# Optimization experiments

Measured on AMD Instinct MI355X. Metric: run time of the kernel, lower is better.

Reference implementation:

```python
import jax, jax.numpy as jnp
import numpy as np

LR = 0.01
EPS = 1e-10


def setup_inputs() -> dict:
    key = jax.random.key(0)
    k1, k2, k3, k4 = jax.random.split(key, 4)
    N, V, D = 262144, 1000000, 64
    idx = jax.random.randint(k1, (N,), 0, V, dtype=jnp.int64 if jax.config.jax_enable_x64 else jnp.int32)
    grad = jax.random.normal(k2, (N, D), dtype=jnp.float32)
    state = jax.random.uniform(k3, (V, D), dtype=jnp.float32)  # accumulated squared grads (>=0)
    emb = jax.random.normal(k4, (V, D), dtype=jnp.float32)
    return {"idx": idx, "grad": grad, "state": state, "emb": emb}


def reference(idx, grad, state, emb):
    N, D = grad.shape
    V = state.shape[0]
    # unique + segment-mean of grads per unique index (torch.unique + index_add / counts)
    # fixed-size unique for jit; padded slots get fill_value=V (out of range -> dropped on scatter)
    uniq, inverse, counts = jnp.unique(idx, return_inverse=True, return_counts=True,
                                       size=N, fill_value=V)
    grad_sum = jnp.zeros((N, D), dtype=grad.dtype).at[inverse].add(grad)
    grad_values = grad_sum / jnp.maximum(counts, 1)[:, None].astype(grad.dtype)
    # gather state rows (padded rows clip-gather but their writes are dropped)
    state_value = state[jnp.minimum(uniq, V - 1)] + grad_values * grad_values
    new_state = state.at[uniq].set(state_value, mode='drop')
    std_values = jnp.sqrt(state_value) + EPS
    new_emb = emb.at[uniq].add(-(LR * grad_values / std_values), mode='drop')
    return new_state, new_emb
```

## Files before the change

### kernel.cpp

```cpp
#include <hip/hip_runtime.h>

#define LR 0.01f
#define EPS 1e-10f


__global__ void init_head_kernel(int* __restrict__ head, int V) {
    int i = blockIdx.x * blockDim.x + threadIdx.x;
    if (i < V) head[i] = -1;
}

__global__ void link_kernel(const int* __restrict__ idx,
                            int* __restrict__ head,
                            int* __restrict__ next, int N) {
    int i = blockIdx.x * blockDim.x + threadIdx.x;
    if (i >= N) return;
    next[i] = atomicExch(&head[idx[i]], i);
}

__global__ void fused_kernel(const float* __restrict__ state,
                             const float* __restrict__ emb,
                             const float* __restrict__ grad,
                             const int* __restrict__ head,
                             const int* __restrict__ next,
                             float* __restrict__ out_state,
                             float* __restrict__ out_emb, int V) {
    long long t = (long long)blockIdx.x * blockDim.x + threadIdx.x;
    long long row = t >> 4;
    int q = (int)(t & 15);
    if (row >= V) return;
    size_t off = (size_t)row * 64 + (size_t)q * 4;

    int h = head[row];
    float4 s = *reinterpret_cast<const float4*>(state + off);
    float4 e = *reinterpret_cast<const float4*>(emb + off);

    if (h < 0) {
        *reinterpret_cast<float4*>(out_state + off) = s;
        *reinterpret_cast<float4*>(out_emb + off) = e;
        return;
    }

    float sum0 = 0.f, sum1 = 0.f, sum2 = 0.f, sum3 = 0.f;
    int c = 0;
    for (int j = h; j >= 0; j = next[j]) {
        const float4 g = *reinterpret_cast<const float4*>(grad + (size_t)j * 64 + (size_t)q * 4);
        sum0 += g.x; sum1 += g.y; sum2 += g.z; sum3 += g.w;
        ++c;
    }
    float inv = 1.0f / (float)c;
    float m0 = sum0 * inv, m1 = sum1 * inv, m2 = sum2 * inv, m3 = sum3 * inv;
    float s0 = s.x + m0 * m0, s1 = s.y + m1 * m1;
    float s2 = s.z + m2 * m2, s3 = s.w + m3 * m3;
    float4 ns = make_float4(s0, s1, s2, s3);
    float4 ne = make_float4(e.x - LR * m0 / (sqrtf(s0) + EPS),
                            e.y - LR * m1 / (sqrtf(s1) + EPS),
                            e.z - LR * m2 / (sqrtf(s2) + EPS),
                            e.w - LR * m3 / (sqrtf(s3) + EPS));
    *reinterpret_cast<float4*>(out_state + off) = ns;
    *reinterpret_cast<float4*>(out_emb + off) = ne;
}

extern "C" void kernel_launch(void* const* d_in, const int* in_sizes, int n_in,
                              void* d_out, int out_size, void* d_ws, size_t ws_size,
                              hipStream_t stream) {
    const int* idx = (const int*)d_in[0];
    const float* grad = (const float*)d_in[1];
    const float* state = (const float*)d_in[2];
    const float* emb = (const float*)d_in[3];

    int N = in_sizes[0];
    int D = in_sizes[1] / N;
    long long VD = in_sizes[2];
    int V = (int)(VD / D);

    float* out_state = (float*)d_out;
    float* out_emb = (float*)d_out + (size_t)V * D;
    int* head = (int*)d_ws;
    int* next = (int*)d_ws + V;

    const int threads = 256;

    init_head_kernel<<<(V + threads - 1) / threads, threads, 0, stream>>>(head, V);

    link_kernel<<<(N + threads - 1) / threads, threads, 0, stream>>>(idx, head, next, N);

    {
        long long work = (long long)V * 16;
        int blocks = (int)((work + threads - 1) / threads);
        fused_kernel<<<blocks, threads, 0, stream>>>(state, emb, grad, head, next,
                                                     out_state, out_emb, V);
    }
}
```

Before: 214.4 us.

## Use nontemporal loads/stores, grid-stride loop, and memset for head init

Replaces the head-initialisation kernel with hipMemsetAsync. The fused kernel becomes a grid-stride loop with a fixed 4096 blocks. The early-exit branch for untouched rows is removed in favour of a branchless path guarded by c>0. State and embedding rows now use nontemporal vector loads and stores so the streaming traffic does not pollute cache. The aim is to cut launch overhead and cache thrash on a bandwidth-bound pass. The risks are that the fixed grid under-occupies the GPU and that nontemporal hints may not help.

```diff
diff --git a/kernel.cpp b/kernel.cpp
--- a/kernel.cpp
+++ b/kernel.cpp
@@ -3,11 +3,8 @@
 #define LR 0.01f
 #define EPS 1e-10f
 
+typedef float f32x4 __attribute__((ext_vector_type(4)));
 
-__global__ void init_head_kernel(int* __restrict__ head, int V) {
-    int i = blockIdx.x * blockDim.x + threadIdx.x;
-    if (i < V) head[i] = -1;
-}
 
 __global__ void link_kernel(const int* __restrict__ idx,
                             int* __restrict__ head,
@@ -23,41 +20,37 @@
                              const int* __restrict__ head,
                              const int* __restrict__ next,
                              float* __restrict__ out_state,
-                             float* __restrict__ out_emb, int V) {
-    long long t = (long long)blockIdx.x * blockDim.x + threadIdx.x;
-    long long row = t >> 4;
-    int q = (int)(t & 15);
-    if (row >= V) return;
-    size_t off = (size_t)row * 64 + (size_t)q * 4;
+                             float* __restrict__ out_emb, long long total) {
+    long long stride = (long long)gridDim.x * blockDim.x;
+    for (long long t = (long long)blockIdx.x * blockDim.x + threadIdx.x;
+         t < total; t += stride) {
+        long long row = t >> 4;
+        int q = (int)(t & 15);
+        size_t off = (size_t)row * 64 + (size_t)q * 4;
 
-    int h = head[row];
-    float4 s = *reinterpret_cast<const float4*>(state + off);
-    float4 e = *reinterpret_cast<const float4*>(emb + off);
+        int h = head[row];
+        f32x4 s = __builtin_nontemporal_load(reinterpret_cast<const f32x4*>(state + off));
+        f32x4 e = __builtin_nontemporal_load(reinterpret_cast<const f32x4*>(emb + off));
 
-    if (h < 0) {
-        *reinterpret_cast<float4*>(out_state + off) = s;
-        *reinterpret_cast<float4*>(out_emb + off) = e;
-        return;
+        float sum0 = 0.f, sum1 = 0.f, sum2 = 0.f, sum3 = 0.f;
+        int c = 0;
+        for (int j = h; j >= 0; j = next[j]) {
+            const f32x4 g = *reinterpret_cast<const f32x4*>(grad + (size_t)j * 64 + (size_t)q * 4);
+            sum0 += g.x; sum1 += g.y; sum2 += g.z; sum3 += g.w;
+            ++c;
+        }
+        float inv = (c > 0) ? (1.0f / (float)c) : 0.0f;
+        float m0 = sum0 * inv, m1 = sum1 * inv, m2 = sum2 * inv, m3 = sum3 * inv;
+        float s0 = s.x + m0 * m0, s1 = s.y + m1 * m1;
+        float s2 = s.z + m2 * m2, s3 = s.w + m3 * m3;
+        f32x4 ns = { s0, s1, s2, s3 };
+        f32x4 ne = { e.x - LR * m0 / (sqrtf(s0) + EPS),
+                     e.y - LR * m1 / (sqrtf(s1) + EPS),
+                     e.z - LR * m2 / (sqrtf(s2) + EPS),
+                     e.w - LR * m3 / (sqrtf(s3) + EPS) };
+        __builtin_nontemporal_store(ns, reinterpret_cast<f32x4*>(out_state + off));
+        __builtin_nontemporal_store(ne, reinterpret_cast<f32x4*>(out_emb + off));
     }
-
-    float sum0 = 0.f, sum1 = 0.f, sum2 = 0.f, sum3 = 0.f;
-    int c = 0;
-    for (int j = h; j >= 0; j = next[j]) {
-        const float4 g = *reinterpret_cast<const float4*>(grad + (size_t)j * 64 + (size_t)q * 4);
-        sum0 += g.x; sum1 += g.y; sum2 += g.z; sum3 += g.w;
-        ++c;
-    }
-    float inv = 1.0f / (float)c;
-    float m0 = sum0 * inv, m1 = sum1 * inv, m2 = sum2 * inv, m3 = sum3 * inv;
-    float s0 = s.x + m0 * m0, s1 = s.y + m1 * m1;
-    float s2 = s.z + m2 * m2, s3 = s.w + m3 * m3;
-    float4 ns = make_float4(s0, s1, s2, s3);
-    float4 ne = make_float4(e.x - LR * m0 / (sqrtf(s0) + EPS),
-                            e.y - LR * m1 / (sqrtf(s1) + EPS),
-                            e.z - LR * m2 / (sqrtf(s2) + EPS),
-                            e.w - LR * m3 / (sqrtf(s3) + EPS));
-    *reinterpret_cast<float4*>(out_state + off) = ns;
-    *reinterpret_cast<float4*>(out_emb + off) = ne;
 }
 
 extern "C" void kernel_launch(void* const* d_in, const int* in_sizes, int n_in,
@@ -80,14 +73,14 @@
 
     const int threads = 256;
 
-    init_head_kernel<<<(V + threads - 1) / threads, threads, 0, stream>>>(head, V);
+    (void)hipMemsetAsync(head, 0xFF, (size_t)V * sizeof(int), stream);
 
     link_kernel<<<(N + threads - 1) / threads, threads, 0, stream>>>(idx, head, next, N);
 
     {
-        long long work = (long long)V * 16;
-        int blocks = (int)((work + threads - 1) / threads);
+        long long total = (long long)V * 16;
+        int blocks = 4096;
         fused_kernel<<<blocks, threads, 0, stream>>>(state, emb, grad, head, next,
-                                                     out_state, out_emb, V);
+                                                     out_state, out_emb, total);
     }
 }
```

New measurement: 219.4 us. +2.3%, slower.
